# Kernel tuning notes

Hardware: AMD Instinct MI355X
Metric: run time of the kernel (lower is better)

The kernel has to match this reference:

```python
import jax, jax.numpy as jnp
import numpy as np
from jax import lax

C = 128  # channels after deconv_2

def _deconvs(x, w1, b1, w2, b2):
    # x: (N,512,4,4)
    N = x.shape[0]
    # ConvTranspose2d k=1 s=2: 4 -> 7; values land on even positions, bias elsewhere
    z1 = jnp.einsum('nchw,co->nohw', x, w1)  # (N,256,4,4)
    h1 = jnp.broadcast_to(b1[None, :, None, None], (N, 256, 7, 7))
    h1 = h1.at[:, :, ::2, ::2].set(z1 + b1[None, :, None, None])
    # ConvTranspose2d k=1 s=2 pad=1: 7 -> 11; full output 13 at even idx, crop 1 each side
    # -> input positions 1..5 land at output odd positions 1,3,5,7,9
    z2 = jnp.einsum('nchw,co->nohw', h1, w2)  # (N,128,7,7)
    feat = jnp.broadcast_to(b2[None, :, None, None], (N, C, 11, 11))
    feat = feat.at[:, :, 1::2, 1::2].set(z2[:, :, 1:6, 1:6] + b2[None, :, None, None])
    return feat  # (N,128,11,11)

def _categorize(rois):
    r = rois.astype(jnp.int32)
    y0, x0, y1, x1 = r[:, 0], r[:, 1], r[:, 2], r[:, 3]
    inb = jnp.all((r >= 0) & (r < 11), axis=1)
    h, w = y1 - y0, x1 - x0
    cat = jnp.where(inb & (h == 4) & (w == 4), 0,
          jnp.where(inb & (h == 8) & (w == 8), 1,
          jnp.where(inb & (h == 4) & (w == 8), 2,
          jnp.where(inb & (h == 6) & (w == 8), 3, 4))))
    # invalid anchors -> forced crop (1,1,10,10) i.e. 9x9 starting at (1,1)
    y0 = jnp.where(cat == 4, 1, y0)
    x0 = jnp.where(cat == 4, 1, x0)
    return y0, x0, cat

def _pool_one(f, y0, x0, cat):
    # f: (128,11,11); compute all 5 pooling candidates, select by category
    neg = jnp.finfo(f.dtype).min
    c0 = lax.dynamic_slice(f, (0, y0, x0), (C, 4, 4))                    # identity
    s88 = lax.dynamic_slice(f, (0, y0, x0), (C, 8, 8))
    c1 = s88.reshape(C, 4, 2, 4, 2).max(axis=(2, 4))                    # 2x2 s2
    s48 = lax.dynamic_slice(f, (0, y0, x0), (C, 4, 8))
    c2 = s48.reshape(C, 4, 4, 2).max(axis=3)                            # 1d pool k2
    s68 = lax.dynamic_slice(f, (0, y0, x0), (C, 6, 8))
    p68 = jnp.pad(s68, ((0, 0), (1, 1), (0, 0)), constant_values=neg)   # pad H by 1
    c3 = p68.reshape(C, 4, 2, 4, 2).max(axis=(2, 4))                    # 2x2 s2 padH1
    s99 = lax.dynamic_slice(f, (0, y0, x0), (C, 9, 9))
    c4 = lax.reduce_window(s99, neg, lax.max, (1, 3, 3), (1, 2, 2), 'VALID')  # 3x3 s2
    return jnp.stack([c0, c1, c2, c3, c4])[cat]

def reference(base_feat, rois, w1, b1, w2, b2, wl, bl):
    B = base_feat.shape[0]
    x = base_feat.reshape(-1, 512, 4, 4)
    feat = _deconvs(x, w1, b1, w2, b2)          # (N,128,11,11)
    y0, x0, cat = _categorize(rois)
    pooled = jax.vmap(_pool_one)(feat, y0, x0, cat)   # (N,128,4,4)
    h = pooled.reshape(B, -1, 2048) @ wl + bl         # (B,R,1024)
    return jnp.where(h > 0, h, 0.01 * h)              # LeakyReLU(0.01)

def setup_inputs():
    key = jax.random.key(0)
    ks = jax.random.split(key, 8)
    B, R = 32, 256
    N = B * R
    return {
        'base_feat': jax.random.normal(ks[0], (B, R, 512, 4, 4), jnp.float32),
        'rois': jax.random.randint(ks[1], (N, 4), 0, 12, jnp.int32),
        'w1': jax.random.normal(ks[2], (512, 256), jnp.float32) * 0.02,
        'b1': jax.random.normal(ks[3], (256,), jnp.float32) * 0.02,
        'w2': jax.random.normal(ks[4], (256, 128), jnp.float32) * 0.02,
        'b2': jax.random.normal(ks[5], (128,), jnp.float32) * 0.02,
        'wl': jax.random.normal(ks[6], (2048, 1024), jnp.float32) * 0.02,
        'bl': jax.random.normal(ks[7], (1024,), jnp.float32) * 0.02,
    }
```

## Files before the change

### kernel.cpp

```cpp
#include <hip/hip_runtime.h>
#include <float.h>
#include <stdint.h>

typedef __attribute__((ext_vector_type(8))) short bf16x8;
typedef __attribute__((ext_vector_type(4))) float f32x4;

__device__ __forceinline__ unsigned short f2bf(float f) {
  unsigned u = __builtin_bit_cast(unsigned, f);
  u += 0x7fffu + ((u >> 16) & 1u);
  return (unsigned short)(u >> 16);
}

__device__ __forceinline__ void gl_lds16(const void* g, void* s) {
  __builtin_amdgcn_global_load_lds(
      (const __attribute__((address_space(1))) unsigned int*)(uintptr_t)g,
      (__attribute__((address_space(3))) unsigned int*)(unsigned int)(uintptr_t)s,
      16, 0, 0);
}

__device__ __forceinline__ int cellmask(int cat, int y0, int x0, int i, int j) {
  int ys[3], xs[3];
  int ny, nx;
  switch (cat) {
    case 0: ys[0] = y0 + i; ny = 1; xs[0] = x0 + j; nx = 1; break;
    case 1: ys[0] = y0 + 2 * i; ys[1] = ys[0] + 1; ny = 2;
            xs[0] = x0 + 2 * j; xs[1] = xs[0] + 1; nx = 2; break;
    case 2: ys[0] = y0 + i; ny = 1;
            xs[0] = x0 + 2 * j; xs[1] = xs[0] + 1; nx = 2; break;
    case 3: if (i == 0) { ys[0] = y0; ny = 1; }
            else if (i == 3) { ys[0] = y0 + 5; ny = 1; }
            else { ys[0] = y0 + 2 * i - 1; ys[1] = y0 + 2 * i; ny = 2; }
            xs[0] = x0 + 2 * j; xs[1] = xs[0] + 1; nx = 2; break;
    default: ys[0] = 1 + 2 * i; ys[1] = 2 + 2 * i; ys[2] = 3 + 2 * i; ny = 3;
             xs[0] = 1 + 2 * j; xs[1] = 2 + 2 * j; xs[2] = 3 + 2 * j; nx = 3; break;
  }
  int m = 0;
  for (int a = 0; a < ny; ++a)
    for (int b = 0; b < nx; ++b) {
      int y = ys[a], xx = xs[b];
      if ((y & 1) && (xx & 1)) {
        if ((y == 3 || y == 7) && (xx == 3 || xx == 7))
          m |= 1 << (2 + ((y == 7) ? 2 : 0) + ((xx == 7) ? 1 : 0));
        else
          m |= 2;
      } else {
        m |= 1;
      }
    }
  return m;
}

__global__ __launch_bounds__(256) void k_prep(
    const float* __restrict__ w1, const float* __restrict__ b1,
    const float* __restrict__ w2, const float* __restrict__ b2,
    const float* __restrict__ wl, const int* __restrict__ rois,
    unsigned short* __restrict__ Wt, float* __restrict__ dval,
    unsigned char* __restrict__ masks, unsigned short* __restrict__ wlT)
{
  __shared__ float tile[64][65];
  const int blk = blockIdx.x;
  const int t = threadIdx.x;
  if (blk < 512) {
    int c = blk & 15;
    int o0 = ((blk >> 4) & 1) * 64;
    int m0 = (blk >> 5) * 64;
    int tl = t & 63, th = t >> 6;
    for (int s = 0; s < 16; ++s) {
      int ol = s * 4 + th;
      tile[ol][tl] = wl[((o0 + ol) * 16 + c) * 1024 + m0 + tl];
    }
    __syncthreads();
    for (int s = 0; s < 16; ++s) {
      int ml = s * 4 + th;
      wlT[(size_t)(m0 + ml) * 2048 + c * 128 + o0 + tl] = f2bf(tile[tl][ml]);
    }
  } else if (blk < 576) {
    int tid = (blk - 512) * 256 + t;
    int o = tid & 127;
    int kc = tid >> 7;
    for (int kk = 0; kk < 4; ++kk) {
      int k = kc * 4 + kk;
      const float* w1r = w1 + k * 256;
      float a0 = 0.f, a1 = 0.f;
      for (int c = 0; c < 256; c += 2) {
        a0 += w1r[c] * w2[c * 128 + o];
        a1 += w1r[c + 1] * w2[(c + 1) * 128 + o];
      }
      Wt[o * 512 + k] = f2bf(a0 + a1);
    }
  } else if (blk < 608) {
    int n = (blk - 576) * 256 + t;
    const int* rr = rois + n * 4;
    int y0 = rr[0], x0 = rr[1], y1 = rr[2], x1 = rr[3];
    bool inb = ((unsigned)y0 < 11u) && ((unsigned)x0 < 11u) &&
               ((unsigned)y1 < 11u) && ((unsigned)x1 < 11u);
    int h = y1 - y0, ww = x1 - x0;
    int cat;
    if (inb && h == 4 && ww == 4) cat = 0;
    else if (inb && h == 8 && ww == 8) cat = 1;
    else if (inb && h == 4 && ww == 8) cat = 2;
    else if (inb && h == 6 && ww == 8) cat = 3;
    else { cat = 4; y0 = 1; x0 = 1; }
    union { unsigned char b[16]; uint4 q; } u;
    for (int cell = 0; cell < 16; ++cell)
      u.b[cell] = (unsigned char)cellmask(cat, y0, x0, cell >> 2, cell & 3);
    *(uint4*)(masks + n * 16) = u.q;
  } else {
    if (t < 128) {
      float acc = 0.f;
      for (int c = 0; c < 256; ++c) acc += b1[c] * w2[c * 128 + t];
      dval[t] = acc + b2[t];
    }
  }
}

__global__ __launch_bounds__(256) void k_dgemm_pool(
    const float* __restrict__ x,
    const unsigned short* __restrict__ Wt,
    const float* __restrict__ dval, const float* __restrict__ b2,
    const unsigned char* __restrict__ masks,
    unsigned short* __restrict__ pooled)
{
  __shared__ __align__(16) unsigned short As[64 * 64];
  __shared__ __align__(16) unsigned short Bs[128 * 64];
  const int t = threadIdx.x;
  const int bm = blockIdx.x;
  const int n0 = bm * 16;
  const int w = t >> 6, lane = t & 63;
  const int wm = (w >> 1) * 32, wn = (w & 1) * 64;
  const int lrow = lane & 15, lk = (lane >> 4) * 8;

  f32x4 acc[2][4];
  const f32x4 z = {0.f, 0.f, 0.f, 0.f};
  for (int i = 0; i < 2; ++i) for (int j = 0; j < 4; ++j) acc[i][j] = z;

  const int brow = t >> 1, bhalf = (t & 1) * 32;
  for (int k0 = 0; k0 < 512; k0 += 64) {
    {
      const unsigned short* gp = Wt + brow * 512 + k0 + bhalf;
      uint4 q0 = *(const uint4*)(gp + 0);
      uint4 q1 = *(const uint4*)(gp + 8);
      uint4 q2 = *(const uint4*)(gp + 16);
      uint4 q3 = *(const uint4*)(gp + 24);
      unsigned short* sp = Bs + brow * 64 + bhalf;
      *(uint4*)(sp + 0)  = q0;
      *(uint4*)(sp + 8)  = q1;
      *(uint4*)(sp + 16) = q2;
      *(uint4*)(sp + 24) = q3;
    }
#pragma unroll
    for (int s = 0; s < 4; ++s) {
      int li = s * 256 + t;
      int nl = li >> 6;
      int k = li & 63;
      const float* gp = x + (size_t)(n0 + nl) * 8192 + (size_t)(k0 + k) * 16;
      float4 qa = *(const float4*)(gp + 4);
      float4 qb = *(const float4*)(gp + 8);
      unsigned short* sp = As + nl * 256 + k;
      sp[0]   = f2bf(qa.y);
      sp[64]  = f2bf(qa.z);
      sp[128] = f2bf(qb.y);
      sp[192] = f2bf(qb.z);
    }
    __syncthreads();
#pragma unroll
    for (int kk = 0; kk < 64; kk += 32) {
      bf16x8 a[2], b[4];
      for (int i = 0; i < 2; ++i)
        a[i] = *(const bf16x8*)&As[(wm + i * 16 + lrow) * 64 + kk + lk];
      for (int j = 0; j < 4; ++j)
        b[j] = *(const bf16x8*)&Bs[(wn + j * 16 + lrow) * 64 + kk + lk];
      for (int i = 0; i < 2; ++i)
        for (int j = 0; j < 4; ++j)
          acc[i][j] = __builtin_amdgcn_mfma_f32_16x16x32_bf16(a[i], b[j], acc[i][j], 0, 0, 0);
    }
    __syncthreads();
  }

  const int lr = lane >> 4, lc = lane & 15;
  for (int i = 0; i < 2; ++i) {
    int n = n0 + (wm >> 2) + i * 4 + lr;
    uint4 mq = *(const uint4*)(masks + n * 16);
    const unsigned char* mb = (const unsigned char*)&mq;
    for (int j = 0; j < 4; ++j) {
      int o = wn + j * 16 + lc;
      float dv = dval[o], bv = b2[o];
      float d0 = acc[i][j][0] + dv, d1 = acc[i][j][1] + dv;
      float d2 = acc[i][j][2] + dv, d3 = acc[i][j][3] + dv;
      unsigned short* op = pooled + (size_t)n * 2048 + o;
#pragma unroll
      for (int cell = 0; cell < 16; ++cell) {
        int m = mb[cell];
        float v = (m & 1) ? bv : -FLT_MAX;
        if (m & 2)  v = fmaxf(v, dv);
        if (m & 4)  v = fmaxf(v, d0);
        if (m & 8)  v = fmaxf(v, d1);
        if (m & 16) v = fmaxf(v, d2);
        if (m & 32) v = fmaxf(v, d3);
        op[cell * 128] = f2bf(v);
      }
    }
  }
}

__global__ __launch_bounds__(256) void k_gemm(
    const unsigned short* __restrict__ A,
    const unsigned short* __restrict__ B,
    const float* __restrict__ bias,
    float* __restrict__ C)
{
  __shared__ __align__(16) unsigned short As[128 * 64];
  __shared__ __align__(16) unsigned short Bs[128 * 64];
  const int t = threadIdx.x;
  const int r0 = blockIdx.x * 128, c0 = blockIdx.y * 128;
  const int w = t >> 6, lane = t & 63;
  const int wm = (w >> 1) * 64, wn = (w & 1) * 64;
  const int lrow = lane & 15, lk = (lane >> 4) * 8;

  f32x4 acc[4][4];
  const f32x4 z = {0.f, 0.f, 0.f, 0.f};
  for (int i = 0; i < 4; ++i) for (int j = 0; j < 4; ++j) acc[i][j] = z;

  const int srow = lane >> 3;
  const int scol = ((lane & 7) ^ srow) * 8;
  const unsigned short* Ag = A + (size_t)(r0 + w * 32 + srow) * 2048 + scol;
  const unsigned short* Bg = B + (size_t)(c0 + w * 32 + srow) * 2048 + scol;
  unsigned short* Asb = As + (w * 32) * 64;
  unsigned short* Bsb = Bs + (w * 32) * 64;

  int sw[2][4];
#pragma unroll
  for (int kh = 0; kh < 2; ++kh)
#pragma unroll
    for (int q = 0; q < 4; ++q)
      sw[kh][q] = (((kh * 4 + q) ^ (lrow & 7)) * 8);

  const int myq = lk >> 3;

  for (int k0 = 0; k0 < 2048; k0 += 64) {
#pragma unroll
    for (int c = 0; c < 4; ++c) {
      gl_lds16(Ag + (size_t)c * 8 * 2048 + k0, Asb + c * 8 * 64);
      gl_lds16(Bg + (size_t)c * 8 * 2048 + k0, Bsb + c * 8 * 64);
    }
    __syncthreads();
#pragma unroll
    for (int kk = 0; kk < 64; kk += 32) {
      const int off = sw[kk >> 5][myq];
      bf16x8 a[4], b[4];
      for (int i = 0; i < 4; ++i)
        a[i] = *(const bf16x8*)&As[(wm + i * 16 + lrow) * 64 + off];
      for (int j = 0; j < 4; ++j)
        b[j] = *(const bf16x8*)&Bs[(wn + j * 16 + lrow) * 64 + off];
      for (int i = 0; i < 4; ++i)
        for (int j = 0; j < 4; ++j)
          acc[i][j] = __builtin_amdgcn_mfma_f32_16x16x32_bf16(a[i], b[j], acc[i][j], 0, 0, 0);
    }
    __syncthreads();
  }

  const int rbase = r0 + wm + (lane >> 4) * 4;
  for (int j = 0; j < 4; ++j) {
    int col = c0 + wn + j * 16 + (lane & 15);
    float bv = bias[col];
    for (int i = 0; i < 4; ++i) {
      for (int r = 0; r < 4; ++r) {
        int row = rbase + i * 16 + r;
        float v = acc[i][j][r] + bv;
        C[(size_t)row * 1024 + col] = v > 0.f ? v : 0.01f * v;
      }
    }
  }
}

extern "C" void kernel_launch(void* const* d_in, const int* in_sizes, int n_in,
                              void* d_out, int out_size, void* d_ws, size_t ws_size,
                              hipStream_t stream) {
  const float* base_feat = (const float*)d_in[0];
  const int*   rois      = (const int*)d_in[1];
  const float* w1        = (const float*)d_in[2];
  const float* b1        = (const float*)d_in[3];
  const float* w2        = (const float*)d_in[4];
  const float* b2        = (const float*)d_in[5];
  const float* wl        = (const float*)d_in[6];
  const float* bl        = (const float*)d_in[7];
  float* out = (float*)d_out;

  char* ws = (char*)d_ws;
  unsigned short* Wt     = (unsigned short*)(ws + 0);
  float*          dval   = (float*)(ws + 131072);
  unsigned char*  masks  = (unsigned char*)(ws + 131584);
  unsigned short* pooled = (unsigned short*)(ws + 262656);
  unsigned short* wlT    = (unsigned short*)(ws + 33817088);

  k_prep      <<<dim3(609),  dim3(256), 0, stream>>>(w1, b1, w2, b2, wl, rois,
                                                     Wt, dval, masks, wlT);
  k_dgemm_pool<<<dim3(512),  dim3(256), 0, stream>>>(base_feat, Wt, dval, b2, masks, pooled);
  k_gemm      <<<dim3(64, 8), dim3(256), 0, stream>>>(pooled, wlT, bl, out);
}
```

Baseline: 500.8 us.

## Move wl transpose into main dgemm-pool kernel to overlap with feature compute

The wl transpose/bf16 conversion blocks move out of the prep kernel and into the main deconv-GEMM+pool kernel, interleaved as odd block indices. The prep kernel becomes small (weight fold and masks only), so its critical path shortens, and the memory-bound transpose runs concurrently with the compute-heavy dgemm blocks. Shared memory is unified into one raw buffer aliased by both roles. The cost is a larger grid in the main kernel and possible contention between the two block types.

Result: slower. 521.7 us (+4.2%).

```diff
diff --git a/kernel.cpp b/kernel.cpp
--- a/kernel.cpp
+++ b/kernel.cpp
@@ -50,32 +50,17 @@
   return m;
 }
 
-__global__ __launch_bounds__(256) void k_prep(
+__global__ __launch_bounds__(256) void k_prep0(
     const float* __restrict__ w1, const float* __restrict__ b1,
     const float* __restrict__ w2, const float* __restrict__ b2,
-    const float* __restrict__ wl, const int* __restrict__ rois,
+    const int* __restrict__ rois,
     unsigned short* __restrict__ Wt, float* __restrict__ dval,
-    unsigned char* __restrict__ masks, unsigned short* __restrict__ wlT)
+    unsigned char* __restrict__ masks)
 {
-  __shared__ float tile[64][65];
   const int blk = blockIdx.x;
   const int t = threadIdx.x;
-  if (blk < 512) {
-    int c = blk & 15;
-    int o0 = ((blk >> 4) & 1) * 64;
-    int m0 = (blk >> 5) * 64;
-    int tl = t & 63, th = t >> 6;
-    for (int s = 0; s < 16; ++s) {
-      int ol = s * 4 + th;
-      tile[ol][tl] = wl[((o0 + ol) * 16 + c) * 1024 + m0 + tl];
-    }
-    __syncthreads();
-    for (int s = 0; s < 16; ++s) {
-      int ml = s * 4 + th;
-      wlT[(size_t)(m0 + ml) * 2048 + c * 128 + o0 + tl] = f2bf(tile[tl][ml]);
-    }
-  } else if (blk < 576) {
-    int tid = (blk - 512) * 256 + t;
+  if (blk < 64) {
+    int tid = blk * 256 + t;
     int o = tid & 127;
     int kc = tid >> 7;
     for (int kk = 0; kk < 4; ++kk) {
@@ -88,8 +73,8 @@
       }
       Wt[o * 512 + k] = f2bf(a0 + a1);
     }
-  } else if (blk < 608) {
-    int n = (blk - 576) * 256 + t;
+  } else if (blk < 96) {
+    int n = (blk - 64) * 256 + t;
     const int* rr = rois + n * 4;
     int y0 = rr[0], x0 = rr[1], y1 = rr[2], x1 = rr[3];
     bool inb = ((unsigned)y0 < 11u) && ((unsigned)x0 < 11u) &&
@@ -114,17 +99,41 @@
   }
 }
 
-__global__ __launch_bounds__(256) void k_dgemm_pool(
+__global__ __launch_bounds__(256) void k_main(
     const float* __restrict__ x,
     const unsigned short* __restrict__ Wt,
     const float* __restrict__ dval, const float* __restrict__ b2,
     const unsigned char* __restrict__ masks,
-    unsigned short* __restrict__ pooled)
+    const float* __restrict__ wl,
+    unsigned short* __restrict__ pooled,
+    unsigned short* __restrict__ wlT)
 {
-  __shared__ __align__(16) unsigned short As[64 * 64];
-  __shared__ __align__(16) unsigned short Bs[128 * 64];
+  __shared__ __align__(16) char smraw[24576];
+  const int blk = blockIdx.x;
   const int t = threadIdx.x;
-  const int bm = blockIdx.x;
+
+  if (blk & 1) {
+    float (*tile)[65] = (float(*)[65])smraw;
+    int b = blk >> 1;
+    int c = b & 15;
+    int o0 = ((b >> 4) & 1) * 64;
+    int m0 = (b >> 5) * 64;
+    int tl = t & 63, th = t >> 6;
+    for (int s = 0; s < 16; ++s) {
+      int ol = s * 4 + th;
+      tile[ol][tl] = wl[((o0 + ol) * 16 + c) * 1024 + m0 + tl];
+    }
+    __syncthreads();
+    for (int s = 0; s < 16; ++s) {
+      int ml = s * 4 + th;
+      wlT[(size_t)(m0 + ml) * 2048 + c * 128 + o0 + tl] = f2bf(tile[tl][ml]);
+    }
+    return;
+  }
+
+  unsigned short* As = (unsigned short*)smraw;
+  unsigned short* Bs = (unsigned short*)(smraw + 8192);
+  const int bm = blk >> 1;
   const int n0 = bm * 16;
   const int w = t >> 6, lane = t & 63;
   const int wm = (w >> 1) * 32, wn = (w & 1) * 64;
@@ -293,8 +302,8 @@
   unsigned short* pooled = (unsigned short*)(ws + 262656);
   unsigned short* wlT    = (unsigned short*)(ws + 33817088);
 
-  k_prep      <<<dim3(609),  dim3(256), 0, stream>>>(w1, b1, w2, b2, wl, rois,
-                                                     Wt, dval, masks, wlT);
-  k_dgemm_pool<<<dim3(512),  dim3(256), 0, stream>>>(base_feat, Wt, dval, b2, masks, pooled);
-  k_gemm      <<<dim3(64, 8), dim3(256), 0, stream>>>(pooled, wlT, bl, out);
-}
+  k_prep0<<<dim3(97),   dim3(256), 0, stream>>>(w1, b1, w2, b2, rois, Wt, dval, masks);
+  k_main <<<dim3(1024), dim3(256), 0, stream>>>(base_feat, Wt, dval, b2, masks, wl,
+                                                pooled, wlT);
+  k_gemm <<<dim3(64, 8), dim3(256), 0, stream>>>(pooled, wlT, bl, out);
+}
```
